# Kernel optimization log

Hardware: AMD Instinct MI355X
Metric: run time of the kernel (lower is better)

Reference implementation:

```python
import jax, jax.numpy as jnp
import numpy as np

NUM_GRAPHS = 64
EPS = 1e-6


def setup_inputs() -> dict:
    key = jax.random.key(0)
    ks = jax.random.split(key, 16)
    S, B, IN, H, N, P_IN, P_OUT = 256, 64, 3, 128, 1_000_000, 8, 32
    src = jax.random.normal(ks[0], (S, B, IN), dtype=jnp.float32)
    src_len = jnp.maximum(jax.random.randint(ks[1], (B,), 0, S + 1), 1).astype(jnp.int32)
    node_x = jax.random.normal(ks[2], (N, H), dtype=jnp.float32)
    # w is a 0/1 node validity mask in the original (float)
    node_w = (jax.random.uniform(ks[3], (N,)) < 0.9).astype(jnp.float32)
    graph_ids = jnp.sort(jax.random.randint(ks[4], (N,), 0, NUM_GRAPHS)).astype(jnp.int32)
    pro_features = jax.random.normal(ks[5], (B, P_IN), dtype=jnp.float32)
    s_in = 1.0 / np.sqrt(IN)
    s_h = 1.0 / np.sqrt(H)
    s_p = 1.0 / np.sqrt(P_IN)
    s_c = 1.0 / np.sqrt(H + P_OUT)
    W_in = jax.random.uniform(ks[6], (IN, H), minval=-s_in, maxval=s_in)
    b_in = jax.random.uniform(ks[7], (H,), minval=-s_in, maxval=s_in)
    W_pred = jax.random.uniform(ks[8], (H, 1), minval=-s_h, maxval=s_h)
    b_pred = jax.random.uniform(ks[9], (1,), minval=-s_h, maxval=s_h)
    W_extra = jax.random.uniform(ks[10], (P_IN, P_OUT), minval=-s_p, maxval=s_p)
    b_extra = jax.random.uniform(ks[11], (P_OUT,), minval=-s_p, maxval=s_p)
    W_hid = jax.random.uniform(ks[12], (P_OUT + H, H), minval=-s_c, maxval=s_c)
    b_hid = jax.random.uniform(ks[13], (H,), minval=-s_c, maxval=s_c)
    return {"src": src, "src_len": src_len, "node_x": node_x, "node_w": node_w,
            "graph_ids": graph_ids, "pro_features": pro_features,
            "W_in": W_in, "b_in": b_in, "W_pred": W_pred, "b_pred": b_pred,
            "W_extra": W_extra, "b_extra": b_extra, "W_hid": W_hid, "b_hid": b_hid}


def mask_graph_log_softmax(lg, w, graph_ids):
    # lg: [N], w: [N], graph_ids: [N] sorted segment ids -> per-graph masked softmax, then log
    maxes = jax.ops.segment_max(lg, graph_ids, num_segments=NUM_GRAPHS)
    x_exp = jnp.exp(lg - maxes[graph_ids]) * w
    x_sum = jax.ops.segment_sum(x_exp, graph_ids, num_segments=NUM_GRAPHS)
    pred = x_exp / (x_sum[graph_ids] + EPS)
    return jnp.log(jnp.clip(pred, EPS, 1.0))


def reference(src, src_len, node_x, node_w, graph_ids, pro_features,
              W_in, b_in, W_pred, b_pred, W_extra, b_extra, W_hid, b_hid):
    S, B = src.shape[0], src.shape[1]
    # mask2d[i, t] = 1 for t < src_len[i]
    mask2d = (jnp.arange(S)[None, :] < src_len[:, None]).astype(src.dtype)  # [B, S]
    h = jnp.tanh(0.0) + src @ W_in + b_in  # [S, B, H]  (fc_in; transformer treated as identity)
    # zero out padded timesteps, then mean over dim 0 (torch.mean divides by S)
    outputs = h * mask2d.T[:, :, None]  # [S, B, H]
    hidden = jnp.mean(outputs, axis=0, keepdims=True)  # [1, B, H]
    # graph segment softmax on node scores
    lg = (node_x @ W_pred + b_pred)[:, 0]  # [N]
    lg_out = mask_graph_log_softmax(lg, node_w, graph_ids)[:, None]  # [N, 1]
    # pro feature fusion
    extra_emb = jnp.tanh(pro_features @ W_extra + b_extra)[None]  # [1, B, P_OUT]
    hidden = jnp.tanh(jnp.concatenate((extra_emb, hidden), axis=2) @ W_hid + b_hid)  # [1, B, H]
    return outputs, hidden, lg_out
```

## Files before the change

kernel.cpp:

```cpp
#include <hip/hip_runtime.h>

#define S_DIM 256
#define B_DIM 64
#define IN_DIM 3
#define H_DIM 128
#define N_NODES 1000000
#define P_INF 8
#define P_OUTF 32
#define NUM_GRAPHS 64
#define EPSF 1e-6f

#define OUT_OUTPUTS 0
#define OUT_HIDDEN (S_DIM * B_DIM * H_DIM)
#define OUT_LG (OUT_HIDDEN + B_DIM * H_DIM)

#define NBLK 2048
#define RPB 489
#define RPW 123
#define SG_SLOTS 6

#define WS_HIDPART 0
#define WS_TBLV (8 * B_DIM * H_DIM)
#define WS_TBLG (WS_TBLV + NBLK * SG_SLOTS)

__global__ void __launch_bounds__(256)
main_kernel(const float* __restrict__ src, const int* __restrict__ src_len,
            const float* __restrict__ W_in, const float* __restrict__ b_in,
            const float* __restrict__ node_x, const float* __restrict__ W_pred,
            const float* __restrict__ b_pred, const float* __restrict__ node_w,
            const int* __restrict__ gids,
            float* __restrict__ outputs, float* __restrict__ hid_partial,
            float* __restrict__ lg, float* __restrict__ tblV, int* __restrict__ tblG) {
    __shared__ float sg[SG_SLOTS];
    const int tid = threadIdx.x;
    const int blk = blockIdx.x;
    if (tid < SG_SLOTS) sg[tid] = 0.0f;

    if (blk < 256) {
        int b = blk & 63;
        int chunk = blk >> 6;
        int h = tid & 127;
        int shalf = tid >> 7;
        float w0 = W_in[h], w1 = W_in[H_DIM + h], w2 = W_in[2 * H_DIM + h];
        float bi = b_in[h];
        int len = src_len[b];
        float facc = 0.0f;
        int s0 = chunk * 64 + shalf * 32;
        for (int s = s0; s < s0 + 32; ++s) {
            const float* sp = src + ((size_t)s * B_DIM + b) * IN_DIM;
            float v = fmaf(sp[0], w0, fmaf(sp[1], w1, fmaf(sp[2], w2, bi)));
            v = (s < len) ? v : 0.0f;
            outputs[((size_t)s * B_DIM + b) * H_DIM + h] = v;
            facc += v;
        }
        hid_partial[((size_t)(chunk * 2 + shalf) * B_DIM + b) * H_DIM + h] = facc;
    }
    __syncthreads();

    const int start = blk * RPB;
    const int bend = min(start + RPB, N_NODES);
    const int gfirst = (start < N_NODES) ? gids[start] : 0;
    const int wid = tid >> 6;
    const int lane = tid & 63;
    const int half = lane >> 5;
    const int sub = lane & 31;
    const int wstart = start + wid * RPW;
    const int wend = min(wstart + RPW, bend);
    float4 w4 = ((const float4*)W_pred)[sub];
    float bp = b_pred[0];
    int curg = -1;
    float acc = 0.0f;
    for (int r0 = wstart; r0 < wend; r0 += 8) {
        float4 x[4];
        #pragma unroll
        for (int k = 0; k < 4; ++k) {
            int row = r0 + 2 * k + half;
            x[k] = (row < wend) ? ((const float4*)(node_x + (size_t)row * H_DIM))[sub]
                                : make_float4(0.f, 0.f, 0.f, 0.f);
        }
        float s[4];
        #pragma unroll
        for (int k = 0; k < 4; ++k)
            s[k] = x[k].x * w4.x + x[k].y * w4.y + x[k].z * w4.z + x[k].w * w4.w;
        #pragma unroll
        for (int off = 1; off < 32; off <<= 1) {
            #pragma unroll
            for (int k = 0; k < 4; ++k) s[k] += __shfl_xor(s[k], off);
        }
        if (sub == 0) {
            #pragma unroll
            for (int k = 0; k < 4; ++k) {
                int row = r0 + 2 * k + half;
                if (row < wend) {
                    float score = s[k] + bp;
                    lg[row] = score;
                    float xe = expf(score) * node_w[row];
                    int g = gids[row];
                    if (g != curg) {
                        if (curg >= 0) atomicAdd(&sg[min(curg - gfirst, SG_SLOTS - 1)], acc);
                        curg = g;
                        acc = 0.0f;
                    }
                    acc += xe;
                }
            }
        }
    }
    if (sub == 0 && curg >= 0) atomicAdd(&sg[min(curg - gfirst, SG_SLOTS - 1)], acc);
    __syncthreads();
    if (tid < SG_SLOTS) tblV[blk * SG_SLOTS + tid] = sg[tid];
    if (tid == 0) tblG[blk] = gfirst;
}

#define LGOUT_BLOCKS 977

__global__ void __launch_bounds__(256)
finish_kernel(const float* __restrict__ tblV, const int* __restrict__ tblG,
              float* __restrict__ lg, const int* __restrict__ gids,
              const float* __restrict__ node_w,
              const float* __restrict__ pro, const float* __restrict__ W_extra,
              const float* __restrict__ b_extra, const float* __restrict__ W_hid,
              const float* __restrict__ b_hid, const float* __restrict__ hid_partial,
              float* __restrict__ hidden_out) {
    const int tid = threadIdx.x;
    const int blk = blockIdx.x;

    if (blk >= LGOUT_BLOCKS) {
        int b = blk - LGOUT_BLOCKS;
        __shared__ float sh[P_OUTF + H_DIM];
        if (tid < P_OUTF) {
            float a = b_extra[tid];
            #pragma unroll
            for (int k = 0; k < P_INF; ++k) a += pro[b * P_INF + k] * W_extra[k * P_OUTF + tid];
            sh[tid] = tanhf(a);
        }
        if (tid < H_DIM) {
            float m = 0.0f;
            #pragma unroll
            for (int c = 0; c < 8; ++c) m += hid_partial[((size_t)c * B_DIM + b) * H_DIM + tid];
            sh[P_OUTF + tid] = m * (1.0f / S_DIM);
        }
        __syncthreads();
        if (tid < H_DIM) {
            float a = b_hid[tid];
            #pragma unroll 8
            for (int k = 0; k < P_OUTF + H_DIM; ++k) a += sh[k] * W_hid[k * H_DIM + tid];
            hidden_out[(size_t)b * H_DIM + tid] = tanhf(a);
        }
        return;
    }

    __shared__ float gsum[NUM_GRAPHS];
    if (tid < NUM_GRAPHS) gsum[tid] = 0.0f;
    __syncthreads();
    {
        int curg = -1;
        float a = 0.0f;
        for (int b = tid * (NBLK / 256); b < (tid + 1) * (NBLK / 256); ++b) {
            int gf = tblG[b];
            #pragma unroll
            for (int slot = 0; slot < SG_SLOTS; ++slot) {
                float v = tblV[b * SG_SLOTS + slot];
                if (v != 0.0f) {
                    int g = min(gf + slot, NUM_GRAPHS - 1);
                    if (g != curg) {
                        if (curg >= 0) atomicAdd(&gsum[curg], a);
                        curg = g;
                        a = 0.0f;
                    }
                    a += v;
                }
            }
        }
        if (curg >= 0) atomicAdd(&gsum[curg], a);
    }
    __syncthreads();

    int n4 = blk * 256 + tid;
    if (n4 >= N_NODES / 4) return;
    float4 l = ((const float4*)lg)[n4];
    float4 w = ((const float4*)node_w)[n4];
    int4 g = ((const int4*)gids)[n4];
    float4 r;
    r.x = logf(fminf(fmaxf(expf(l.x) * w.x / (gsum[g.x] + EPSF), EPSF), 1.0f));
    r.y = logf(fminf(fmaxf(expf(l.y) * w.y / (gsum[g.y] + EPSF), EPSF), 1.0f));
    r.z = logf(fminf(fmaxf(expf(l.z) * w.z / (gsum[g.z] + EPSF), EPSF), 1.0f));
    r.w = logf(fminf(fmaxf(expf(l.w) * w.w / (gsum[g.w] + EPSF), EPSF), 1.0f));
    ((float4*)lg)[n4] = r;
}

extern "C" void kernel_launch(void* const* d_in, const int* in_sizes, int n_in,
                              void* d_out, int out_size, void* d_ws, size_t ws_size,
                              hipStream_t stream) {
    const float* src      = (const float*)d_in[0];
    const int*   src_len  = (const int*)d_in[1];
    const float* node_x   = (const float*)d_in[2];
    const float* node_w   = (const float*)d_in[3];
    const int*   gids     = (const int*)d_in[4];
    const float* pro      = (const float*)d_in[5];
    const float* W_in     = (const float*)d_in[6];
    const float* b_in     = (const float*)d_in[7];
    const float* W_pred   = (const float*)d_in[8];
    const float* b_pred   = (const float*)d_in[9];
    const float* W_extra  = (const float*)d_in[10];
    const float* b_extra  = (const float*)d_in[11];
    const float* W_hid    = (const float*)d_in[12];
    const float* b_hid    = (const float*)d_in[13];

    float* out = (float*)d_out;
    float* outputs = out + OUT_OUTPUTS;
    float* hidden  = out + OUT_HIDDEN;
    float* lg      = out + OUT_LG;

    float* ws = (float*)d_ws;
    float* hid_partial = ws + WS_HIDPART;
    float* tblV = ws + WS_TBLV;
    int*   tblG = (int*)(ws + WS_TBLG);

    main_kernel<<<NBLK, 256, 0, stream>>>(src, src_len, W_in, b_in,
                                          node_x, W_pred, b_pred, node_w, gids,
                                          outputs, hid_partial, lg, tblV, tblG);

    finish_kernel<<<LGOUT_BLOCKS + B_DIM, 256, 0, stream>>>(tblV, tblG, lg, gids, node_w,
                                                            pro, W_extra, b_extra, W_hid,
                                                            b_hid, hid_partial, hidden);
}
```

Before: 144.9 us.

## Fuse main and finish kernels into one cooperative kernel with grid sync

Merges the node-scoring/partial-sum kernel and the finish kernel into a single cooperative launch. A grid-wide barrier separates the segment-sum reduction from the log-softmax pass. The grid is halved to 1024 blocks with more rows per block, and launch bounds request 4 blocks per CU so all blocks can be co-resident. This removes one kernel launch and the gap between kernels, and each block rereads its own slice of lg, which may still be in cache. The costs are grid-sync overhead, the requirement that every block fit on the device at once, and fewer blocks to hide memory latency in the bandwidth-bound node_x pass.

```diff
diff --git a/kernel.cpp b/kernel.cpp
--- a/kernel.cpp
+++ b/kernel.cpp
@@ -1,4 +1,7 @@
 #include <hip/hip_runtime.h>
+#include <hip/hip_cooperative_groups.h>
+
+namespace cg = cooperative_groups;
 
 #define S_DIM 256
 #define B_DIM 64
@@ -14,24 +17,33 @@
 #define OUT_HIDDEN (S_DIM * B_DIM * H_DIM)
 #define OUT_LG (OUT_HIDDEN + B_DIM * H_DIM)
 
-#define NBLK 2048
-#define RPB 489
-#define RPW 123
+#define NBLK 1024
+#define RPB 977
+#define RPW 245
 #define SG_SLOTS 6
+#define N4_TOTAL (N_NODES / 4)
+#define N4_PER_BLK 245
+#define FUSION_BASE 512
 
 #define WS_HIDPART 0
 #define WS_TBLV (8 * B_DIM * H_DIM)
 #define WS_TBLG (WS_TBLV + NBLK * SG_SLOTS)
 
-__global__ void __launch_bounds__(256)
-main_kernel(const float* __restrict__ src, const int* __restrict__ src_len,
-            const float* __restrict__ W_in, const float* __restrict__ b_in,
-            const float* __restrict__ node_x, const float* __restrict__ W_pred,
-            const float* __restrict__ b_pred, const float* __restrict__ node_w,
-            const int* __restrict__ gids,
-            float* __restrict__ outputs, float* __restrict__ hid_partial,
-            float* __restrict__ lg, float* __restrict__ tblV, int* __restrict__ tblG) {
+__global__ void __launch_bounds__(256, 4)
+fused_kernel(const float* __restrict__ src, const int* __restrict__ src_len,
+             const float* __restrict__ W_in, const float* __restrict__ b_in,
+             const float* __restrict__ node_x, const float* __restrict__ W_pred,
+             const float* __restrict__ b_pred, const float* __restrict__ node_w,
+             const int* __restrict__ gids,
+             const float* __restrict__ pro, const float* __restrict__ W_extra,
+             const float* __restrict__ b_extra, const float* __restrict__ W_hid,
+             const float* __restrict__ b_hid,
+             float* __restrict__ outputs, float* __restrict__ hidden_out,
+             float* __restrict__ lg, float* __restrict__ hid_partial,
+             float* __restrict__ tblV, int* __restrict__ tblG) {
     __shared__ float sg[SG_SLOTS];
+    __shared__ float gsum[NUM_GRAPHS];
+    __shared__ float sh[P_OUTF + H_DIM];
     const int tid = threadIdx.x;
     const int blk = blockIdx.x;
     if (tid < SG_SLOTS) sg[tid] = 0.0f;
@@ -59,7 +71,7 @@
 
     const int start = blk * RPB;
     const int bend = min(start + RPB, N_NODES);
-    const int gfirst = (start < N_NODES) ? gids[start] : 0;
+    const int gfirst = gids[start];
     const int wid = tid >> 6;
     const int lane = tid & 63;
     const int half = lane >> 5;
@@ -110,24 +122,52 @@
     __syncthreads();
     if (tid < SG_SLOTS) tblV[blk * SG_SLOTS + tid] = sg[tid];
     if (tid == 0) tblG[blk] = gfirst;
-}
-
-#define LGOUT_BLOCKS 977
-
-__global__ void __launch_bounds__(256)
-finish_kernel(const float* __restrict__ tblV, const int* __restrict__ tblG,
-              float* __restrict__ lg, const int* __restrict__ gids,
-              const float* __restrict__ node_w,
-              const float* __restrict__ pro, const float* __restrict__ W_extra,
-              const float* __restrict__ b_extra, const float* __restrict__ W_hid,
-              const float* __restrict__ b_hid, const float* __restrict__ hid_partial,
-              float* __restrict__ hidden_out) {
-    const int tid = threadIdx.x;
-    const int blk = blockIdx.x;
-
-    if (blk >= LGOUT_BLOCKS) {
-        int b = blk - LGOUT_BLOCKS;
-        __shared__ float sh[P_OUTF + H_DIM];
+
+    cg::this_grid().sync();
+
+    if (tid < NUM_GRAPHS) gsum[tid] = 0.0f;
+    __syncthreads();
+    {
+        int cg2 = -1;
+        float a = 0.0f;
+        #pragma unroll
+        for (int b = tid * (NBLK / 256); b < (tid + 1) * (NBLK / 256); ++b) {
+            int gf = tblG[b];
+            #pragma unroll
+            for (int slot = 0; slot < SG_SLOTS; ++slot) {
+                float v = tblV[b * SG_SLOTS + slot];
+                if (v != 0.0f) {
+                    int g = min(gf + slot, NUM_GRAPHS - 1);
+                    if (g != cg2) {
+                        if (cg2 >= 0) atomicAdd(&gsum[cg2], a);
+                        cg2 = g;
+                        a = 0.0f;
+                    }
+                    a += v;
+                }
+            }
+        }
+        if (cg2 >= 0) atomicAdd(&gsum[cg2], a);
+    }
+    __syncthreads();
+
+    if (tid < N4_PER_BLK) {
+        int n4 = blk * N4_PER_BLK + tid;
+        if (n4 < N4_TOTAL) {
+            float4 l = ((const float4*)lg)[n4];
+            float4 w = ((const float4*)node_w)[n4];
+            int4 g = ((const int4*)gids)[n4];
+            float4 r;
+            r.x = logf(fminf(fmaxf(expf(l.x) * w.x / (gsum[g.x] + EPSF), EPSF), 1.0f));
+            r.y = logf(fminf(fmaxf(expf(l.y) * w.y / (gsum[g.y] + EPSF), EPSF), 1.0f));
+            r.z = logf(fminf(fmaxf(expf(l.z) * w.z / (gsum[g.z] + EPSF), EPSF), 1.0f));
+            r.w = logf(fminf(fmaxf(expf(l.w) * w.w / (gsum[g.w] + EPSF), EPSF), 1.0f));
+            ((float4*)lg)[n4] = r;
+        }
+    }
+
+    if (blk >= FUSION_BASE && blk < FUSION_BASE + B_DIM) {
+        int b = blk - FUSION_BASE;
         if (tid < P_OUTF) {
             float a = b_extra[tid];
             #pragma unroll
@@ -147,46 +187,7 @@
             for (int k = 0; k < P_OUTF + H_DIM; ++k) a += sh[k] * W_hid[k * H_DIM + tid];
             hidden_out[(size_t)b * H_DIM + tid] = tanhf(a);
         }
-        return;
-    }
-
-    __shared__ float gsum[NUM_GRAPHS];
-    if (tid < NUM_GRAPHS) gsum[tid] = 0.0f;
-    __syncthreads();
-    {
-        int curg = -1;
-        float a = 0.0f;
-        for (int b = tid * (NBLK / 256); b < (tid + 1) * (NBLK / 256); ++b) {
-            int gf = tblG[b];
-            #pragma unroll
-            for (int slot = 0; slot < SG_SLOTS; ++slot) {
-                float v = tblV[b * SG_SLOTS + slot];
-                if (v != 0.0f) {
-                    int g = min(gf + slot, NUM_GRAPHS - 1);
-                    if (g != curg) {
-                        if (curg >= 0) atomicAdd(&gsum[curg], a);
-                        curg = g;
-                        a = 0.0f;
-                    }
-                    a += v;
-                }
-            }
-        }
-        if (curg >= 0) atomicAdd(&gsum[curg], a);
-    }
-    __syncthreads();
-
-    int n4 = blk * 256 + tid;
-    if (n4 >= N_NODES / 4) return;
-    float4 l = ((const float4*)lg)[n4];
-    float4 w = ((const float4*)node_w)[n4];
-    int4 g = ((const int4*)gids)[n4];
-    float4 r;
-    r.x = logf(fminf(fmaxf(expf(l.x) * w.x / (gsum[g.x] + EPSF), EPSF), 1.0f));
-    r.y = logf(fminf(fmaxf(expf(l.y) * w.y / (gsum[g.y] + EPSF), EPSF), 1.0f));
-    r.z = logf(fminf(fmaxf(expf(l.z) * w.z / (gsum[g.z] + EPSF), EPSF), 1.0f));
-    r.w = logf(fminf(fmaxf(expf(l.w) * w.w / (gsum[g.w] + EPSF), EPSF), 1.0f));
-    ((float4*)lg)[n4] = r;
+    }
 }
 
 extern "C" void kernel_launch(void* const* d_in, const int* in_sizes, int n_in,
@@ -217,11 +218,14 @@
     float* tblV = ws + WS_TBLV;
     int*   tblG = (int*)(ws + WS_TBLG);
 
-    main_kernel<<<NBLK, 256, 0, stream>>>(src, src_len, W_in, b_in,
-                                          node_x, W_pred, b_pred, node_w, gids,
-                                          outputs, hid_partial, lg, tblV, tblG);
-
-    finish_kernel<<<LGOUT_BLOCKS + B_DIM, 256, 0, stream>>>(tblV, tblG, lg, gids, node_w,
-                                                            pro, W_extra, b_extra, W_hid,
-                                                            b_hid, hid_partial, hidden);
+    void* args[] = {
+        (void*)&src, (void*)&src_len, (void*)&W_in, (void*)&b_in,
+        (void*)&node_x, (void*)&W_pred, (void*)&b_pred, (void*)&node_w,
+        (void*)&gids, (void*)&pro, (void*)&W_extra, (void*)&b_extra,
+        (void*)&W_hid, (void*)&b_hid,
+        (void*)&outputs, (void*)&hidden, (void*)&lg, (void*)&hid_partial,
+        (void*)&tblV, (void*)&tblG
+    };
+    hipLaunchCooperativeKernel((const void*)fused_kernel, dim3(NBLK), dim3(256),
+                               args, 0, stream);
 }
```

Measured after the change: 292.0 us. 2.02x slower.
